# Optimization experiments

Hardware: AMD Instinct MI355X
Metric: run time of the kernel (lower is better)

Reference implementation:

```python
import jax, jax.numpy as jnp
import numpy as np

LEAKY = 0.1


def _leaky(x):
    return jnp.where(x > 0, x, LEAKY * x)


def _weightnet(d_xyz, ws):
    # d_xyz: [B,N,K,3]; ws: list of (w [Cin,Cout], b [Cout]) -> [B,N,K,W]
    h = d_xyz
    for w, b in ws:
        h = jax.nn.relu(jnp.einsum('bnki,io->bnko', h, w) + b)
    return h


def _gather(pts, idx):
    # pts: [B,M,C], idx: [B,N,K] -> [B,N,K,C]
    return jax.vmap(lambda p, i: p[i])(pts, idx)


def _cross(xyz1, xyz2, p1, p2, wn, lw, lb, nsample):
    # xyz1 [B,N1,3], xyz2 [B,N2,3], p1 [B,N1,D1], p2 [B,N2,D2]
    B, N1, _ = xyz1.shape
    # squared distances [B,N1,N2]
    d = (jnp.sum(xyz1 ** 2, -1)[:, :, None]
         + jnp.sum(xyz2 ** 2, -1)[:, None, :]
         - 2.0 * jnp.einsum('bnc,bmc->bnm', xyz1, xyz2))
    _, idx = jax.lax.top_k(-d, nsample)          # [B,N1,K] nearest
    neigh_xyz = _gather(xyz2, idx)               # [B,N1,K,3]
    direction = neigh_xyz - xyz1[:, :, None, :]  # [B,N1,K,3]
    gp2 = _gather(p2, idx)                       # [B,N1,K,D2]
    gp1 = jnp.broadcast_to(p1[:, :, None, :], (B, N1, nsample, p1.shape[-1]))
    new_pts = jnp.concatenate([gp1, gp2], axis=-1)   # [B,N1,K,D1+D2]
    w = _weightnet(direction, wn)                    # [B,N1,K,W]
    # [B,N1,D,K] @ [B,N1,K,W] -> [B,N1,D,W] -> flatten D-major (matches torch view)
    agg = jnp.einsum('bnkd,bnkw->bndw', new_pts, w).reshape(B, N1, -1)
    return _leaky(agg @ lw + lb)                     # [B,N1,out]


def setup_inputs() -> dict:
    key = jax.random.key(0)
    ks = jax.random.split(key, 20)
    B, N, C, MID, OUT, W = 4, 4096, 64, 128, 128, 16
    s = 0.05
    inp = {
        'pc1': jax.random.normal(ks[0], (B, 3, N), jnp.float32),
        'pc2': jax.random.normal(ks[1], (B, 3, N), jnp.float32),
        'feat1': jax.random.normal(ks[2], (B, C, N), jnp.float32),
        'feat2': jax.random.normal(ks[3], (B, C, N), jnp.float32),
        # WeightNet1: 3->8->8->16 pointwise linears (torch Conv2d 1x1), stored [Cin,Cout]
        'wn1_w0': jax.random.normal(ks[4], (3, 8), jnp.float32) * s,
        'wn1_b0': jnp.zeros((8,), jnp.float32),
        'wn1_w1': jax.random.normal(ks[5], (8, 8), jnp.float32) * s,
        'wn1_b1': jnp.zeros((8,), jnp.float32),
        'wn1_w2': jax.random.normal(ks[6], (8, W), jnp.float32) * s,
        'wn1_b2': jnp.zeros((W,), jnp.float32),
        'lin1_w': jax.random.normal(ks[7], (2 * C * W, MID), jnp.float32) * s,
        'lin1_b': jnp.zeros((MID,), jnp.float32),
        'wn2_w0': jax.random.normal(ks[8], (3, 8), jnp.float32) * s,
        'wn2_b0': jnp.zeros((8,), jnp.float32),
        'wn2_w1': jax.random.normal(ks[9], (8, 8), jnp.float32) * s,
        'wn2_b1': jnp.zeros((8,), jnp.float32),
        'wn2_w2': jax.random.normal(ks[10], (8, W), jnp.float32) * s,
        'wn2_b2': jnp.zeros((W,), jnp.float32),
        'lin2_w': jax.random.normal(ks[11], (2 * MID * W, OUT), jnp.float32) * s,
        'lin2_b': jnp.zeros((OUT,), jnp.float32),
    }
    return inp


def reference(pc1, pc2, feat1, feat2,
              wn1_w0, wn1_b0, wn1_w1, wn1_b1, wn1_w2, wn1_b2, lin1_w, lin1_b,
              wn2_w0, wn2_b0, wn2_w1, wn2_b1, wn2_w2, wn2_b2, lin2_w, lin2_b):
    nsample = 16
    wn1 = [(wn1_w0, wn1_b0), (wn1_w1, wn1_b1), (wn1_w2, wn1_b2)]
    wn2 = [(wn2_w0, wn2_b0), (wn2_w1, wn2_b1), (wn2_w2, wn2_b2)]
    x1 = pc1.transpose(0, 2, 1)   # [B,N,3]
    x2 = pc2.transpose(0, 2, 1)
    p1 = feat1.transpose(0, 2, 1)  # [B,N,C]
    p2 = feat2.transpose(0, 2, 1)
    f1n = _cross(x1, x2, p1, p2, wn1, lin1_w, lin1_b, nsample)   # [B,N1,mid]
    f2n = _cross(x2, x1, p2, p1, wn1, lin1_w, lin1_b, nsample)   # [B,N2,mid]
    f1f = _cross(x1, x2, f1n, f2n, wn2, lin2_w, lin2_b, nsample) # [B,N1,out]
    return (f1n.transpose(0, 2, 1), f2n.transpose(0, 2, 1), f1f.transpose(0, 2, 1))
```

## Files before the change

### kernel.cpp

```cpp
#include <hip/hip_runtime.h>
#include <hip/hip_bf16.h>
#include <cstddef>
#include <cstdint>

typedef __hip_bfloat16 bf16;
typedef __attribute__((ext_vector_type(8))) short bf16x8;
typedef __attribute__((ext_vector_type(4))) float f32x4;

#define NPT 4096
#define BB  4
#define NBR 16
#define WD  16
#define CDIM 64
#define MIDD 128

#define GLD16(g, l) __builtin_amdgcn_global_load_lds( \
    (const __attribute__((address_space(1))) unsigned int*)(const void*)(g), \
    (__attribute__((address_space(3))) unsigned int*)(void*)(l), 16, 0, 0)

__global__ __launch_bounds__(256)
void prep_kernel(const float* __restrict__ feat1, const float* __restrict__ feat2,
                 float* __restrict__ p1pm, bf16* __restrict__ p1b,
                 float* __restrict__ p2pm, bf16* __restrict__ p2b,
                 const float* __restrict__ lin1_w, bf16* __restrict__ b1hi, bf16* __restrict__ b1lo,
                 const float* __restrict__ lin2_w, bf16* __restrict__ b2hi, bf16* __restrict__ b2lo)
{
    __shared__ float t[32][33];
    const int tx = threadIdx.x & 31, ty = threadIdx.x >> 5;
    const int id = blockIdx.x;
    if (id < 2048) {
        const int which = id >> 10;
        const int nt = id & 1023;
        const int n0 = (nt & 127) * 32;
        const int c0 = ((nt >> 7) & 1) * 32;
        const int b  = nt >> 8;
        const float* in = which ? feat2 : feat1;
        float* out  = which ? p2pm : p1pm;
        bf16*  outb = which ? p2b  : p1b;
        #pragma unroll
        for (int r = ty; r < 32; r += 8)
            t[r][tx] = in[((size_t)b * CDIM + c0 + r) * NPT + n0 + tx];
        __syncthreads();
        #pragma unroll
        for (int r = ty; r < 32; r += 8) {
            const float v = t[tx][r];
            out [((size_t)b * NPT + n0 + r) * CDIM + c0 + tx] = v;
            outb[((size_t)b * NPT + n0 + r) * CDIM + c0 + tx] = __float2bfloat16(v);
        }
    } else {
        const float* w; bf16 *hi, *lo; int K, k0, o0;
        if (id < 2304) {
            const int id2 = id - 2048;
            w = lin1_w; hi = b1hi; lo = b1lo; K = 2048;
            k0 = (id2 & 63) * 32; o0 = (id2 >> 6) * 32;
        } else {
            const int id2 = id - 2304;
            w = lin2_w; hi = b2hi; lo = b2lo; K = 4096;
            k0 = (id2 & 127) * 32; o0 = (id2 >> 7) * 32;
        }
        #pragma unroll
        for (int r = ty; r < 32; r += 8)
            t[r][tx] = w[(size_t)(k0 + r) * MIDD + o0 + tx];
        __syncthreads();
        #pragma unroll
        for (int r = ty; r < 32; r += 8) {
            const float v = t[tx][r];
            const bf16 h = __float2bfloat16(v);
            const bf16 l2 = __float2bfloat16(v - __bfloat162float(h));
            hi[(size_t)(o0 + r) * K + k0 + tx] = h;
            lo[(size_t)(o0 + r) * K + k0 + tx] = l2;
        }
    }
}

#define KQ     16
#define KSEG   16
#define KCH    64
#define KSTAGE 1024
#define KRING  96

__global__ __launch_bounds__(256)
void knn_kernel(const float* __restrict__ pcA, const float* __restrict__ pcB,
                int* __restrict__ idxAB, int* __restrict__ idxBA)
{
    const float *qxyz, *cxyz; int* idx_out;
    if (blockIdx.z == 0) { qxyz = pcA; cxyz = pcB; idx_out = idxAB; }
    else                 { qxyz = pcB; cxyz = pcA; idx_out = idxBA; }

    __shared__ float4 cf[KSTAGE + KSTAGE / KCH];
    __shared__ float  pubd[2][KSEG][KQ];
    __shared__ float4 qc[KQ];
    __shared__ float  u16s[KQ];
    __shared__ int    rcnt[KQ];
    __shared__ int    wtot;
    __shared__ int    wl[256];
    __shared__ float  ringd[KQ][KRING + 1];
    __shared__ int    ringi[KQ][KRING + 1];

    const int tid = threadIdx.x;
    const int q   = tid & (KQ - 1);
    const int s   = tid >> 4;
    const int b   = blockIdx.y;
    const int n   = blockIdx.x * KQ + q;

    const float* qp = qxyz + (size_t)b * 3 * NPT;
    const float qx = qp[n], qy = qp[NPT + n], qz = qp[2 * NPT + n];
    const float q2 = fmaf(qx, qx, fmaf(qy, qy, qz * qz));
    const float* c = cxyz + (size_t)b * 3 * NPT;

    if (tid < KQ) rcnt[tid] = 0;
    if (tid == 0) wtot = 0;
    if (s == 0) qc[q] = make_float4(qx, qy, qz, q2);

    float b0 = 3.4e38f, b1 = 3.4e38f;
    int   i0 = 0;
    for (int st = 0; st < NPT; st += KSTAGE) {
        __syncthreads();
        {
            #pragma unroll
            for (int r = 0; r < KSTAGE / 256; ++r) {
                const int j = r * 256 + tid;
                const int g = st + j;
                const float x = c[g], y = c[NPT + g], z = c[2 * NPT + g];
                cf[j + (j >> 6)] = make_float4(x, y, z,
                    fmaf(x, x, fmaf(y, y, z * z)));
            }
        }
        __syncthreads();
        const int base = s * (KCH + 1);
        const int gidx = st + s * KCH;
        #pragma unroll 4
        for (int jj = 0; jj < KCH; ++jj) {
            const float4 pv = cf[base + jj];
            const float dot = fmaf(qx, pv.x, fmaf(qy, pv.y, qz * pv.z));
            const float d = q2 + pv.w - 2.f * dot;
            i0 = (d < b0) ? (gidx + jj) : i0;
            const float t = fmaxf(b0, d);
            b0 = fminf(b0, d);
            b1 = fminf(b1, t);
        }
    }
    pubd[0][s][q] = b0;
    pubd[1][s][q] = b1;
    __syncthreads();

    {
        float tv[32];
        #pragma unroll
        for (int j = 0; j < 32; ++j) tv[j] = pubd[j >> 4][j & 15][q];
        #pragma unroll
        for (int rep = 0; rep < 2; ++rep) {
            const int j = rep * 16 + s;
            const float vj = pubd[rep][s][q];
            int rank = 0;
            #pragma unroll
            for (int k = 0; k < 32; ++k)
                rank += (tv[k] < vj || (tv[k] == vj && k < j)) ? 1 : 0;
            if (rank == 15) u16s[q] = vj;
        }
    }
    __syncthreads();

    {
        const float gate = u16s[q];
        if (b0 <= gate) {
            if (b1 > gate) {
                const int slot = atomicAdd(&rcnt[q], 1);
                if (slot < KRING) { ringd[q][slot] = b0; ringi[q][slot] = i0; }
            } else {
                const int u = atomicAdd(&wtot, 1);
                wl[u] = (q << 4) | s;
            }
        }
    }
    __syncthreads();

    {
        const int W = wtot;
        const int lu = tid & 15;
        for (int u = tid >> 4; u < W; u += 16) {
            const int qq  = wl[u] >> 4;
            const int seg = wl[u] & 15;
            const float4 qv = qc[qq];
            const float gate = u16s[qq];
            #pragma unroll
            for (int ch = 0; ch < 4; ++ch) {
                const int j = ch * KSTAGE + seg * KCH + lu * 4;
                const float4 xs = *(const float4*)(c + j);
                const float4 ys = *(const float4*)(c + NPT + j);
                const float4 zs = *(const float4*)(c + 2 * NPT + j);
                const float xv[4] = { xs.x, xs.y, xs.z, xs.w };
                const float yv[4] = { ys.x, ys.y, ys.z, ys.w };
                const float zv[4] = { zs.x, zs.y, zs.z, zs.w };
                #pragma unroll
                for (int e = 0; e < 4; ++e) {
                    const float p2 = fmaf(xv[e], xv[e], fmaf(yv[e], yv[e], zv[e] * zv[e]));
                    const float dot = fmaf(qv.x, xv[e], fmaf(qv.y, yv[e], qv.z * zv[e]));
                    const float d = qv.w + p2 - 2.f * dot;
                    if (d <= gate) {
                        const int slot = atomicAdd(&rcnt[qq], 1);
                        if (slot < KRING) { ringd[qq][slot] = d; ringi[qq][slot] = j + e; }
                    }
                }
            }
        }
    }
    __syncthreads();

    {
        const int cnt = min(rcnt[q], KRING);
        int* op = idx_out + ((size_t)b * NPT + n) * NBR;
        for (int e = s; e < cnt; e += KSEG) {
            const float de = ringd[q][e];
            const int   ie = ringi[q][e];
            int rank = 0;
            for (int k = 0; k < cnt; ++k) {
                const float dk = ringd[q][k];
                const int   ik = ringi[q][k];
                rank += (dk < de || (dk == de && ik < ie)) ? 1 : 0;
            }
            if (rank < NBR) op[rank] = ie;
        }
    }
}

template<int D2, int PTS>
__global__ __launch_bounds__(256)
void agg_kernel(const float* __restrict__ qA, const float* __restrict__ cA,
                const bf16* __restrict__ nbrA, const int* __restrict__ idxA,
                const float* __restrict__ qB, const float* __restrict__ cB,
                const bf16* __restrict__ nbrB, const int* __restrict__ idxB,
                int Msplit,
                const float* __restrict__ w0, const float* __restrict__ b0,
                const float* __restrict__ w1, const float* __restrict__ b1,
                const float* __restrict__ w2, const float* __restrict__ b2,
                bf16* __restrict__ agg, float* __restrict__ swb, int m0)
{
    constexpr int TPP  = 256 / PTS;
    constexpr int ND   = D2 / TPP;
    constexpr int WSTR = 276;

    __shared__ float wp[248];
    __shared__ int   nb[PTS * NBR];
    __shared__ float wgt[PTS * WSTR];

    const int tid = threadIdx.x;
    const int mbase = m0 + (int)blockIdx.x * PTS;
    const bool second = mbase >= Msplit;
    const int mrow = second ? mbase - Msplit : mbase;
    const float* qxyz   = second ? qB   : qA;
    const float* cxyz   = second ? cB   : cA;
    const bf16*  nbr_b  = second ? nbrB : nbrA;
    const int*   idx    = second ? idxB : idxA;
    const int b = mrow >> 12;
    const int nbase = mrow & (NPT - 1);

    if (tid < 248) {
        float v;
        if      (tid <  24) v = w0[tid];
        else if (tid <  32) v = b0[tid - 24];
        else if (tid <  96) v = w1[tid - 32];
        else if (tid < 104) v = b1[tid - 96];
        else if (tid < 232) v = w2[tid - 104];
        else                v = b2[tid - 232];
        wp[tid] = v;
    }
    if (tid < PTS * NBR)
        nb[tid] = idx[(size_t)mrow * NBR + tid];
    __syncthreads();

    const int p  = tid & (PTS - 1);
    const int dg = tid / PTS;
    const int d0 = dg * ND;

    unsigned int F[NBR];
    {
        const bf16* base = nbr_b + (size_t)b * NPT * D2 + d0;
        #pragma unroll
        for (int k = 0; k < NBR; ++k) {
            const int j = nb[p * NBR + k];
            F[k] = *(const unsigned int*)(base + (size_t)j * D2);
        }
    }

    if (tid < PTS * NBR) {
        const int pp = tid / NBR, k = tid % NBR;
        const int n = nbase + pp;
        const int j = nb[tid];
        const float* q = qxyz + (size_t)b * 3 * NPT;
        const float* c = cxyz + (size_t)b * 3 * NPT;
        const float dx = c[j]           - q[n];
        const float dy = c[NPT + j]     - q[NPT + n];
        const float dz = c[2 * NPT + j] - q[2 * NPT + n];
        float h1[8], h2[8];
        #pragma unroll
        for (int o = 0; o < 8; ++o) {
            float v = wp[24 + o];
            v = fmaf(dx, wp[o], v);
            v = fmaf(dy, wp[8 + o], v);
            v = fmaf(dz, wp[16 + o], v);
            h1[o] = fmaxf(v, 0.f);
        }
        #pragma unroll
        for (int o = 0; o < 8; ++o) {
            float v = wp[96 + o];
            #pragma unroll
            for (int i = 0; i < 8; ++i) v = fmaf(h1[i], wp[32 + i * 8 + o], v);
            h2[o] = fmaxf(v, 0.f);
        }
        #pragma unroll
        for (int o = 0; o < WD; ++o) {
            float v = wp[232 + o];
            #pragma unroll
            for (int i = 0; i < 8; ++i) v = fmaf(h2[i], wp[104 + i * WD + o], v);
            wgt[pp * WSTR + k * WD + o] = fmaxf(v, 0.f);
        }
    }
    __syncthreads();

    if (tid < PTS * 16) {
        const int pp = tid >> 4, w = tid & 15;
        const float* wgp = wgt + pp * WSTR + w;
        float sv = 0.f;
        #pragma unroll
        for (int k = 0; k < NBR; ++k) sv += wgp[k * WD];
        swb[(size_t)((int)blockIdx.x * PTS + pp) * 16 + w] = sv;
    }

    {
        const float* wg = wgt + p * WSTR;
        bf16* aout = agg + ((size_t)((int)blockIdx.x * PTS + p)) * (2 * D2 * WD);
        float acc[ND][16];
        #pragma unroll
        for (int di = 0; di < ND; ++di)
            #pragma unroll
            for (int w = 0; w < 16; ++w) acc[di][w] = 0.f;
        #pragma unroll
        for (int k = 0; k < NBR; ++k) {
            union { unsigned int u; bf16 h[2]; } uf;
            uf.u = F[k];
            float Fv[ND];
            #pragma unroll
            for (int j = 0; j < ND; ++j) Fv[j] = __bfloat162float(uf.h[j]);
            const float4 v0 = *(const float4*)(wg + k * WD);
            const float4 v1 = *(const float4*)(wg + k * WD + 4);
            const float4 v2 = *(const float4*)(wg + k * WD + 8);
            const float4 v3 = *(const float4*)(wg + k * WD + 12);
            float w16[16];
            w16[0]  = v0.x; w16[1]  = v0.y; w16[2]  = v0.z; w16[3]  = v0.w;
            w16[4]  = v1.x; w16[5]  = v1.y; w16[6]  = v1.z; w16[7]  = v1.w;
            w16[8]  = v2.x; w16[9]  = v2.y; w16[10] = v2.z; w16[11] = v2.w;
            w16[12] = v3.x; w16[13] = v3.y; w16[14] = v3.z; w16[15] = v3.w;
            #pragma unroll
            for (int di = 0; di < ND; ++di)
                #pragma unroll
                for (int w = 0; w < 16; ++w)
                    acc[di][w] = fmaf(Fv[di], w16[w], acc[di][w]);
        }
        #pragma unroll
        for (int di = 0; di < ND; ++di) {
            union { bf16 h[16]; uint4 q[2]; } pk;
            #pragma unroll
            for (int w = 0; w < 16; ++w) pk.h[w] = __float2bfloat16(acc[di][w]);
            bf16* dst = aout + (D2 + d0 + di) * WD;
            *(uint4*)dst       = pk.q[0];
            *(uint4*)(dst + 8) = pk.q[1];
        }
    }
}

template<int BM>
__global__ __launch_bounds__(256)
void gemm_mfma(const bf16* __restrict__ A, const bf16* __restrict__ Bhi,
               const bf16* __restrict__ Blo, const float* __restrict__ bias,
               const float* __restrict__ ownf, const float* __restrict__ swb,
               float* __restrict__ out_t, float* __restrict__ out_pm,
               bf16* __restrict__ out_pmb, int m0, int K)
{
    constexpr int AE   = BM * 32;
    constexpr int BUFE = AE + 8192;
    constexpr int MF   = BM / 32;
    __shared__ __align__(16) char smem[2 * BUFE * 2];
    bf16* lds = (bf16*)smem;

    const int tid  = threadIdx.x;
    const int w    = tid >> 6;
    const int lane = tid & 63;
    const int wr   = w >> 1, wc = w & 1;
    const int mb   = (int)blockIdx.x * BM;
    const int gK   = lane >> 4;
    const int rL   = lane & 15;
    const int D2v  = K / 32;

    const int row_r = tid >> 2;
    const int row_s = row_r < BM ? row_r : BM - 1;
    const int ch_s  = tid & 3;
    const int sch_s = ch_s ^ ((row_s >> 1) & 3);
    const int w0_s  = (sch_s & 1) * 8;
    float sww[8];
    {
        const float* sp = swb + (size_t)(mb + row_s) * 16 + w0_s;
        const float4 a = *(const float4*)sp;
        const float4 b2 = *(const float4*)(sp + 4);
        sww[0] = a.x;  sww[1] = a.y;  sww[2] = a.z;  sww[3] = a.w;
        sww[4] = b2.x; sww[5] = b2.y; sww[6] = b2.z; sww[7] = b2.w;
    }
    const float* ownrow_g = ownf + (size_t)(m0 + mb + row_s) * D2v;

    f32x4 acc[MF][4];
    #pragma unroll
    for (int i = 0; i < MF; ++i)
        #pragma unroll
        for (int j = 0; j < 4; ++j) acc[i][j] = (f32x4)0.f;

    const int nk = K / 32;
    const int nkOwn = nk / 2;

    auto stage = [&](int buf, int kt) {
        const int kb = kt * 32;
        const int bufo = buf * BUFE;
        if (kt < nkOwn) {
            if (tid < BM * 4) {
                const int d = kt * 2 + (sch_s >> 1);
                const float f = ownrow_g[d];
                union { bf16 h[8]; uint4 q; } pk;
                #pragma unroll
                for (int j = 0; j < 8; ++j) pk.h[j] = __float2bfloat16(f * sww[j]);
                *(uint4*)(lds + bufo + tid * 8) = pk.q;
            }
        } else {
            if (w * 64 < BM * 4)
                GLD16(A + (size_t)(mb + row_r) * K + kb + (sch_s << 3),
                      lds + bufo + ((w * 64) << 3));
        }
        #pragma unroll
        for (int i = 0; i < 2; ++i) {
            const int s2 = i * 256 + tid;
            const int row = s2 >> 2, ch = s2 & 3;
            const int sch = ch ^ ((row >> 1) & 3);
            const int wb = (i * 256 + w * 64) << 3;
            GLD16(Bhi + (size_t)row * K + kb + (sch << 3), lds + bufo + AE + wb);
            GLD16(Blo + (size_t)row * K + kb + (sch << 3), lds + bufo + AE + 4096 + wb);
        }
    };

    stage(0, 0);
    __syncthreads();

    for (int kt = 0; kt < nk; ++kt) {
        const int cur = kt & 1;
        if (kt + 1 < nk) stage(cur ^ 1, kt + 1);

        const bf16* la  = lds + cur * BUFE;
        const bf16* lbh = la + AE;
        const bf16* lbl = la + AE + 4096;

        bf16x8 af[MF], bh[4], bl[4];
        #pragma unroll
        for (int mf = 0; mf < MF; ++mf) {
            const int row = wr * (BM / 2) + mf * 16 + rL;
            af[mf] = *(const bf16x8*)(la + row * 32 + ((gK ^ ((row >> 1) & 3)) << 3));
        }
        #pragma unroll
        for (int nf = 0; nf < 4; ++nf) {
            const int col = wc * 64 + nf * 16 + rL;
            const int off = col * 32 + ((gK ^ ((col >> 1) & 3)) << 3);
            bh[nf] = *(const bf16x8*)(lbh + off);
            bl[nf] = *(const bf16x8*)(lbl + off);
        }
        #pragma unroll
        for (int mf = 0; mf < MF; ++mf)
            #pragma unroll
            for (int nf = 0; nf < 4; ++nf) {
                acc[mf][nf] = __builtin_amdgcn_mfma_f32_16x16x32_bf16(af[mf], bh[nf], acc[mf][nf], 0, 0, 0);
                acc[mf][nf] = __builtin_amdgcn_mfma_f32_16x16x32_bf16(af[mf], bl[nf], acc[mf][nf], 0, 0, 0);
            }
        __syncthreads();
    }

    float (*tile)[133] = (float(*)[133])smem;
    #pragma unroll
    for (int mf = 0; mf < MF; ++mf)
        #pragma unroll
        for (int nf = 0; nf < 4; ++nf) {
            const int col = wc * 64 + nf * 16 + rL;
            const float bs = bias[col];
            #pragma unroll
            for (int qq = 0; qq < 4; ++qq) {
                const int rrow = wr * (BM / 2) + mf * 16 + gK * 4 + qq;
                const float v = acc[mf][nf][qq] + bs;
                tile[rrow][col] = v > 0.f ? v : 0.1f * v;
            }
        }
    __syncthreads();

    const int mrow = m0 + mb;
    const int b = mrow >> 12, n0 = mrow & (NPT - 1);
    for (int e = tid; e < BM * MIDD; e += 256) {
        const int o = e / BM, i = e % BM;
        out_t[((size_t)b * MIDD + o) * NPT + n0 + i] = tile[i][o];
    }
    if (out_pm) {
        for (int e = tid; e < BM * MIDD; e += 256) {
            const int i = e >> 7, o = e & 127;
            const float v = tile[i][o];
            out_pm [(size_t)(mrow + i) * MIDD + o] = v;
            out_pmb[(size_t)(mrow + i) * MIDD + o] = __float2bfloat16(v);
        }
    }
}

extern "C" void kernel_launch(void* const* d_in, const int* in_sizes, int n_in,
                              void* d_out, int out_size, void* d_ws, size_t ws_size,
                              hipStream_t stream)
{
    (void)in_sizes; (void)n_in; (void)out_size;
    const float* pc1    = (const float*)d_in[0];
    const float* pc2    = (const float*)d_in[1];
    const float* feat1  = (const float*)d_in[2];
    const float* feat2  = (const float*)d_in[3];
    const float* wn1_w0 = (const float*)d_in[4];
    const float* wn1_b0 = (const float*)d_in[5];
    const float* wn1_w1 = (const float*)d_in[6];
    const float* wn1_b1 = (const float*)d_in[7];
    const float* wn1_w2 = (const float*)d_in[8];
    const float* wn1_b2 = (const float*)d_in[9];
    const float* lin1_w = (const float*)d_in[10];
    const float* lin1_b = (const float*)d_in[11];
    const float* wn2_w0 = (const float*)d_in[12];
    const float* wn2_b0 = (const float*)d_in[13];
    const float* wn2_w1 = (const float*)d_in[14];
    const float* wn2_b1 = (const float*)d_in[15];
    const float* wn2_w2 = (const float*)d_in[16];
    const float* wn2_b2 = (const float*)d_in[17];
    const float* lin2_w = (const float*)d_in[18];
    const float* lin2_b = (const float*)d_in[19];
    float* out = (float*)d_out;

    const int M  = BB * NPT;
    const int M2 = 2 * M;
    const int K1 = 2 * CDIM * WD;
    const int K2 = 2 * MIDD * WD;

    char* ws = (char*)d_ws;
    float* p1pm = (float*)ws;
    float* p2pm = p1pm + (size_t)M * CDIM;
    float* fpm  = p2pm + (size_t)M * CDIM;
    bf16*  p1b  = (bf16*)(fpm + (size_t)M2 * MIDD);
    bf16*  p2b  = p1b + (size_t)M * CDIM;
    bf16*  fb   = p2b + (size_t)M * CDIM;
    int* idx12  = (int*)(fb + (size_t)M2 * MIDD);
    int* idx21  = idx12 + (size_t)M * NBR;
    bf16* b1hi  = (bf16*)(idx21 + (size_t)M * NBR);
    bf16* b1lo  = b1hi + (size_t)MIDD * K1;
    bf16* b2hi  = b1lo + (size_t)MIDD * K1;
    bf16* b2lo  = b2hi + (size_t)MIDD * K2;
    float* swbuf = (float*)(b2lo + (size_t)MIDD * K2);
    bf16* aggbuf = (bf16*)(swbuf + (size_t)(M2 + 64) * 16);
    const size_t used = (size_t)((char*)aggbuf - ws);
    const size_t avail = ws_size > used ? ws_size - used : 0;

    float* f1t = out;
    float* fft = out + 2 * (size_t)BB * MIDD * NPT;

    prep_kernel<<<2816, 256, 0, stream>>>(feat1, feat2, p1pm, p1b, p2pm, p2b,
                                          lin1_w, b1hi, b1lo, lin2_w, b2hi, b2lo);
    knn_kernel<<<dim3(NPT / KQ, BB, 2), 256, 0, stream>>>(pc1, pc2, idx12, idx21);

    auto chunk_rows = [&](int K) -> int {
        long rows = (long)(avail / ((size_t)K * sizeof(bf16)));
        int cm = (int)(rows > M2 ? M2 : rows) & ~127;
        if (cm < 128) cm = 128;
        return cm;
    };

    {
        const int CMr = chunk_rows(K1);
        for (int m0 = 0; m0 < M2; m0 += CMr) {
            const int cm = (M2 - m0 < CMr) ? (M2 - m0) : CMr;
            agg_kernel<CDIM, 8><<<cm / 8, 256, 0, stream>>>(
                pc1, pc2, p2b, idx12,
                pc2, pc1, p1b, idx21, M,
                wn1_w0, wn1_b0, wn1_w1, wn1_b1, wn1_w2, wn1_b2,
                aggbuf, swbuf, m0);
            gemm_mfma<64><<<cm / 64, 256, 0, stream>>>(aggbuf, b1hi, b1lo, lin1_b,
                                                       p1pm, swbuf,
                                                       f1t, fpm, fb, m0, K1);
        }
    }
    {
        const int CMr = chunk_rows(K2);
        for (int m0 = 0; m0 < M; m0 += CMr) {
            const int cm = (M - m0 < CMr) ? (M - m0) : CMr;
            agg_kernel<MIDD, 4><<<cm / 4, 256, 0, stream>>>(
                pc1, pc2, fb + (size_t)M * MIDD, idx12,
                nullptr, nullptr, nullptr, nullptr, M2,
                wn2_w0, wn2_b0, wn2_w1, wn2_b1, wn2_w2, wn2_b2,
                aggbuf, swbuf, m0);
            gemm_mfma<32><<<cm / 32, 256, 0, stream>>>(aggbuf, b2hi, b2lo, lin2_b,
                                                       fpm, swbuf,
                                                       fft, nullptr, nullptr, m0, K2);
        }
    }
}
```

Measured before the change: 316.1 us.

## Merge prep and kNN kernels into one launch; deepen GEMM K-tile to 64

The feature/weight transpose prep kernel and the kNN kernel become a single launch, with block-index ranges picking the role, so the two independent jobs can overlap and one launch is saved. The split-bf16 MFMA GEMM now stages 64-wide K tiles instead of 32, with an XOR swizzle over 8 chunks and two MFMA sub-steps per tile. This halves the number of barrier-separated k-iterations. In exchange it doubles the LDS footprint per buffer, which may reduce occupancy, and the fused kernel's shared memory now includes both roles' arrays.

```diff
diff --git a/kernel.cpp b/kernel.cpp
--- a/kernel.cpp
+++ b/kernel.cpp
@@ -18,61 +18,6 @@
     (const __attribute__((address_space(1))) unsigned int*)(const void*)(g), \
     (__attribute__((address_space(3))) unsigned int*)(void*)(l), 16, 0, 0)
 
-__global__ __launch_bounds__(256)
-void prep_kernel(const float* __restrict__ feat1, const float* __restrict__ feat2,
-                 float* __restrict__ p1pm, bf16* __restrict__ p1b,
-                 float* __restrict__ p2pm, bf16* __restrict__ p2b,
-                 const float* __restrict__ lin1_w, bf16* __restrict__ b1hi, bf16* __restrict__ b1lo,
-                 const float* __restrict__ lin2_w, bf16* __restrict__ b2hi, bf16* __restrict__ b2lo)
-{
-    __shared__ float t[32][33];
-    const int tx = threadIdx.x & 31, ty = threadIdx.x >> 5;
-    const int id = blockIdx.x;
-    if (id < 2048) {
-        const int which = id >> 10;
-        const int nt = id & 1023;
-        const int n0 = (nt & 127) * 32;
-        const int c0 = ((nt >> 7) & 1) * 32;
-        const int b  = nt >> 8;
-        const float* in = which ? feat2 : feat1;
-        float* out  = which ? p2pm : p1pm;
-        bf16*  outb = which ? p2b  : p1b;
-        #pragma unroll
-        for (int r = ty; r < 32; r += 8)
-            t[r][tx] = in[((size_t)b * CDIM + c0 + r) * NPT + n0 + tx];
-        __syncthreads();
-        #pragma unroll
-        for (int r = ty; r < 32; r += 8) {
-            const float v = t[tx][r];
-            out [((size_t)b * NPT + n0 + r) * CDIM + c0 + tx] = v;
-            outb[((size_t)b * NPT + n0 + r) * CDIM + c0 + tx] = __float2bfloat16(v);
-        }
-    } else {
-        const float* w; bf16 *hi, *lo; int K, k0, o0;
-        if (id < 2304) {
-            const int id2 = id - 2048;
-            w = lin1_w; hi = b1hi; lo = b1lo; K = 2048;
-            k0 = (id2 & 63) * 32; o0 = (id2 >> 6) * 32;
-        } else {
-            const int id2 = id - 2304;
-            w = lin2_w; hi = b2hi; lo = b2lo; K = 4096;
-            k0 = (id2 & 127) * 32; o0 = (id2 >> 7) * 32;
-        }
-        #pragma unroll
-        for (int r = ty; r < 32; r += 8)
-            t[r][tx] = w[(size_t)(k0 + r) * MIDD + o0 + tx];
-        __syncthreads();
-        #pragma unroll
-        for (int r = ty; r < 32; r += 8) {
-            const float v = t[tx][r];
-            const bf16 h = __float2bfloat16(v);
-            const bf16 l2 = __float2bfloat16(v - __bfloat162float(h));
-            hi[(size_t)(o0 + r) * K + k0 + tx] = h;
-            lo[(size_t)(o0 + r) * K + k0 + tx] = l2;
-        }
-    }
-}
-
 #define KQ     16
 #define KSEG   16
 #define KCH    64
@@ -80,13 +25,14 @@
 #define KRING  96
 
 __global__ __launch_bounds__(256)
-void knn_kernel(const float* __restrict__ pcA, const float* __restrict__ pcB,
-                int* __restrict__ idxAB, int* __restrict__ idxBA)
+void pre_kernel(const float* __restrict__ pcA, const float* __restrict__ pcB,
+                int* __restrict__ idxAB, int* __restrict__ idxBA,
+                const float* __restrict__ feat1, const float* __restrict__ feat2,
+                float* __restrict__ p1pm, bf16* __restrict__ p1b,
+                float* __restrict__ p2pm, bf16* __restrict__ p2b,
+                const float* __restrict__ lin1_w, bf16* __restrict__ b1hi, bf16* __restrict__ b1lo,
+                const float* __restrict__ lin2_w, bf16* __restrict__ b2hi, bf16* __restrict__ b2lo)
 {
-    const float *qxyz, *cxyz; int* idx_out;
-    if (blockIdx.z == 0) { qxyz = pcA; cxyz = pcB; idx_out = idxAB; }
-    else                 { qxyz = pcB; cxyz = pcA; idx_out = idxBA; }
-
     __shared__ float4 cf[KSTAGE + KSTAGE / KCH];
     __shared__ float  pubd[2][KSEG][KQ];
     __shared__ float4 qc[KQ];
@@ -96,130 +42,187 @@
     __shared__ int    wl[256];
     __shared__ float  ringd[KQ][KRING + 1];
     __shared__ int    ringi[KQ][KRING + 1];
-
+    __shared__ float  t[32][33];
+
+    const int bid = blockIdx.x;
     const int tid = threadIdx.x;
-    const int q   = tid & (KQ - 1);
-    const int s   = tid >> 4;
-    const int b   = blockIdx.y;
-    const int n   = blockIdx.x * KQ + q;
-
-    const float* qp = qxyz + (size_t)b * 3 * NPT;
-    const float qx = qp[n], qy = qp[NPT + n], qz = qp[2 * NPT + n];
-    const float q2 = fmaf(qx, qx, fmaf(qy, qy, qz * qz));
-    const float* c = cxyz + (size_t)b * 3 * NPT;
-
-    if (tid < KQ) rcnt[tid] = 0;
-    if (tid == 0) wtot = 0;
-    if (s == 0) qc[q] = make_float4(qx, qy, qz, q2);
-
-    float b0 = 3.4e38f, b1 = 3.4e38f;
-    int   i0 = 0;
-    for (int st = 0; st < NPT; st += KSTAGE) {
+
+    if (bid < 2048) {
+        const int dir = bid >> 10;
+        const int b   = (bid >> 8) & 3;
+        const int g   = bid & 255;
+        const float* qxyz = dir ? pcB : pcA;
+        const float* cxyz = dir ? pcA : pcB;
+        int* idx_out      = dir ? idxBA : idxAB;
+
+        const int q = tid & (KQ - 1);
+        const int s = tid >> 4;
+        const int n = g * KQ + q;
+
+        const float* qp = qxyz + (size_t)b * 3 * NPT;
+        const float qx = qp[n], qy = qp[NPT + n], qz = qp[2 * NPT + n];
+        const float q2 = fmaf(qx, qx, fmaf(qy, qy, qz * qz));
+        const float* c = cxyz + (size_t)b * 3 * NPT;
+
+        if (tid < KQ) rcnt[tid] = 0;
+        if (tid == 0) wtot = 0;
+        if (s == 0) qc[q] = make_float4(qx, qy, qz, q2);
+
+        float b0 = 3.4e38f, b1 = 3.4e38f;
+        int   i0 = 0;
+        for (int st = 0; st < NPT; st += KSTAGE) {
+            __syncthreads();
+            {
+                #pragma unroll
+                for (int r = 0; r < KSTAGE / 256; ++r) {
+                    const int j = r * 256 + tid;
+                    const int gg = st + j;
+                    const float x = c[gg], y = c[NPT + gg], z = c[2 * NPT + gg];
+                    cf[j + (j >> 6)] = make_float4(x, y, z,
+                        fmaf(x, x, fmaf(y, y, z * z)));
+                }
+            }
+            __syncthreads();
+            const int base = s * (KCH + 1);
+            const int gidx = st + s * KCH;
+            #pragma unroll 4
+            for (int jj = 0; jj < KCH; ++jj) {
+                const float4 pv = cf[base + jj];
+                const float dot = fmaf(qx, pv.x, fmaf(qy, pv.y, qz * pv.z));
+                const float d = q2 + pv.w - 2.f * dot;
+                i0 = (d < b0) ? (gidx + jj) : i0;
+                const float tt = fmaxf(b0, d);
+                b0 = fminf(b0, d);
+                b1 = fminf(b1, tt);
+            }
+        }
+        pubd[0][s][q] = b0;
+        pubd[1][s][q] = b1;
         __syncthreads();
+
         {
-            #pragma unroll
-            for (int r = 0; r < KSTAGE / 256; ++r) {
-                const int j = r * 256 + tid;
-                const int g = st + j;
-                const float x = c[g], y = c[NPT + g], z = c[2 * NPT + g];
-                cf[j + (j >> 6)] = make_float4(x, y, z,
-                    fmaf(x, x, fmaf(y, y, z * z)));
+            float tv[32];
+            #pragma unroll
+            for (int j = 0; j < 32; ++j) tv[j] = pubd[j >> 4][j & 15][q];
+            #pragma unroll
+            for (int rep = 0; rep < 2; ++rep) {
+                const int j = rep * 16 + s;
+                const float vj = pubd[rep][s][q];
+                int rank = 0;
+                #pragma unroll
+                for (int k = 0; k < 32; ++k)
+                    rank += (tv[k] < vj || (tv[k] == vj && k < j)) ? 1 : 0;
+                if (rank == 15) u16s[q] = vj;
             }
         }
         __syncthreads();
-        const int base = s * (KCH + 1);
-        const int gidx = st + s * KCH;
-        #pragma unroll 4
-        for (int jj = 0; jj < KCH; ++jj) {
-            const float4 pv = cf[base + jj];
-            const float dot = fmaf(qx, pv.x, fmaf(qy, pv.y, qz * pv.z));
-            const float d = q2 + pv.w - 2.f * dot;
-            i0 = (d < b0) ? (gidx + jj) : i0;
-            const float t = fmaxf(b0, d);
-            b0 = fminf(b0, d);
-            b1 = fminf(b1, t);
-        }
-    }
-    pubd[0][s][q] = b0;
-    pubd[1][s][q] = b1;
-    __syncthreads();
-
-    {
-        float tv[32];
-        #pragma unroll
-        for (int j = 0; j < 32; ++j) tv[j] = pubd[j >> 4][j & 15][q];
-        #pragma unroll
-        for (int rep = 0; rep < 2; ++rep) {
-            const int j = rep * 16 + s;
-            const float vj = pubd[rep][s][q];
-            int rank = 0;
-            #pragma unroll
-            for (int k = 0; k < 32; ++k)
-                rank += (tv[k] < vj || (tv[k] == vj && k < j)) ? 1 : 0;
-            if (rank == 15) u16s[q] = vj;
-        }
-    }
-    __syncthreads();
-
-    {
-        const float gate = u16s[q];
-        if (b0 <= gate) {
-            if (b1 > gate) {
-                const int slot = atomicAdd(&rcnt[q], 1);
-                if (slot < KRING) { ringd[q][slot] = b0; ringi[q][slot] = i0; }
-            } else {
-                const int u = atomicAdd(&wtot, 1);
-                wl[u] = (q << 4) | s;
-            }
-        }
-    }
-    __syncthreads();
-
-    {
-        const int W = wtot;
-        const int lu = tid & 15;
-        for (int u = tid >> 4; u < W; u += 16) {
-            const int qq  = wl[u] >> 4;
-            const int seg = wl[u] & 15;
-            const float4 qv = qc[qq];
-            const float gate = u16s[qq];
-            #pragma unroll
-            for (int ch = 0; ch < 4; ++ch) {
-                const int j = ch * KSTAGE + seg * KCH + lu * 4;
-                const float4 xs = *(const float4*)(c + j);
-                const float4 ys = *(const float4*)(c + NPT + j);
-                const float4 zs = *(const float4*)(c + 2 * NPT + j);
-                const float xv[4] = { xs.x, xs.y, xs.z, xs.w };
-                const float yv[4] = { ys.x, ys.y, ys.z, ys.w };
-                const float zv[4] = { zs.x, zs.y, zs.z, zs.w };
+
+        {
+            const float gate = u16s[q];
+            if (b0 <= gate) {
+                if (b1 > gate) {
+                    const int slot = atomicAdd(&rcnt[q], 1);
+                    if (slot < KRING) { ringd[q][slot] = b0; ringi[q][slot] = i0; }
+                } else {
+                    const int u = atomicAdd(&wtot, 1);
+                    wl[u] = (q << 4) | s;
+                }
+            }
+        }
+        __syncthreads();
+
+        {
+            const int W = wtot;
+            const int lu = tid & 15;
+            for (int u = tid >> 4; u < W; u += 16) {
+                const int qq  = wl[u] >> 4;
+                const int seg = wl[u] & 15;
+                const float4 qv = qc[qq];
+                const float gate = u16s[qq];
                 #pragma unroll
-                for (int e = 0; e < 4; ++e) {
-                    const float p2 = fmaf(xv[e], xv[e], fmaf(yv[e], yv[e], zv[e] * zv[e]));
-                    const float dot = fmaf(qv.x, xv[e], fmaf(qv.y, yv[e], qv.z * zv[e]));
-                    const float d = qv.w + p2 - 2.f * dot;
-                    if (d <= gate) {
-                        const int slot = atomicAdd(&rcnt[qq], 1);
-                        if (slot < KRING) { ringd[qq][slot] = d; ringi[qq][slot] = j + e; }
+                for (int ch = 0; ch < 4; ++ch) {
+                    const int j = ch * KSTAGE + seg * KCH + lu * 4;
+                    const float4 xs = *(const float4*)(c + j);
+                    const float4 ys = *(const float4*)(c + NPT + j);
+                    const float4 zs = *(const float4*)(c + 2 * NPT + j);
+                    const float xv[4] = { xs.x, xs.y, xs.z, xs.w };
+                    const float yv[4] = { ys.x, ys.y, ys.z, ys.w };
+                    const float zv[4] = { zs.x, zs.y, zs.z, zs.w };
+                    #pragma unroll
+                    for (int e = 0; e < 4; ++e) {
+                        const float p2 = fmaf(xv[e], xv[e], fmaf(yv[e], yv[e], zv[e] * zv[e]));
+                        const float dot = fmaf(qv.x, xv[e], fmaf(qv.y, yv[e], qv.z * zv[e]));
+                        const float d = qv.w + p2 - 2.f * dot;
+                        if (d <= gate) {
+                            const int slot = atomicAdd(&rcnt[qq], 1);
+                            if (slot < KRING) { ringd[qq][slot] = d; ringi[qq][slot] = j + e; }
+                        }
                     }
                 }
             }
         }
-    }
-    __syncthreads();
-
-    {
-        const int cnt = min(rcnt[q], KRING);
-        int* op = idx_out + ((size_t)b * NPT + n) * NBR;
-        for (int e = s; e < cnt; e += KSEG) {
-            const float de = ringd[q][e];
-            const int   ie = ringi[q][e];
-            int rank = 0;
-            for (int k = 0; k < cnt; ++k) {
-                const float dk = ringd[q][k];
-                const int   ik = ringi[q][k];
-                rank += (dk < de || (dk == de && ik < ie)) ? 1 : 0;
-            }
-            if (rank < NBR) op[rank] = ie;
+        __syncthreads();
+
+        {
+            const int cnt = min(rcnt[q], KRING);
+            int* op = idx_out + ((size_t)b * NPT + n) * NBR;
+            for (int e = s; e < cnt; e += KSEG) {
+                const float de = ringd[q][e];
+                const int   ie = ringi[q][e];
+                int rank = 0;
+                for (int k = 0; k < cnt; ++k) {
+                    const float dk = ringd[q][k];
+                    const int   ik = ringi[q][k];
+                    rank += (dk < de || (dk == de && ik < ie)) ? 1 : 0;
+                }
+                if (rank < NBR) op[rank] = ie;
+            }
+        }
+    } else {
+        const int tx = tid & 31, ty = tid >> 5;
+        const int id = bid - 2048;
+        if (id < 2048) {
+            const int which = id >> 10;
+            const int nt = id & 1023;
+            const int n0 = (nt & 127) * 32;
+            const int c0 = ((nt >> 7) & 1) * 32;
+            const int b  = nt >> 8;
+            const float* in = which ? feat2 : feat1;
+            float* out  = which ? p2pm : p1pm;
+            bf16*  outb = which ? p2b  : p1b;
+            #pragma unroll
+            for (int r = ty; r < 32; r += 8)
+                t[r][tx] = in[((size_t)b * CDIM + c0 + r) * NPT + n0 + tx];
+            __syncthreads();
+            #pragma unroll
+            for (int r = ty; r < 32; r += 8) {
+                const float v = t[tx][r];
+                out [((size_t)b * NPT + n0 + r) * CDIM + c0 + tx] = v;
+                outb[((size_t)b * NPT + n0 + r) * CDIM + c0 + tx] = __float2bfloat16(v);
+            }
+        } else {
+            const float* w; bf16 *hi, *lo; int K, k0, o0;
+            if (id < 2304) {
+                const int id2 = id - 2048;
+                w = lin1_w; hi = b1hi; lo = b1lo; K = 2048;
+                k0 = (id2 & 63) * 32; o0 = (id2 >> 6) * 32;
+            } else {
+                const int id2 = id - 2304;
+                w = lin2_w; hi = b2hi; lo = b2lo; K = 4096;
+                k0 = (id2 & 127) * 32; o0 = (id2 >> 7) * 32;
+            }
+            #pragma unroll
+            for (int r = ty; r < 32; r += 8)
+                t[r][tx] = w[(size_t)(k0 + r) * MIDD + o0 + tx];
+            __syncthreads();
+            #pragma unroll
+            for (int r = ty; r < 32; r += 8) {
+                const float v = t[tx][r];
+                const bf16 h = __float2bfloat16(v);
+                const bf16 l2 = __float2bfloat16(v - __bfloat162float(h));
+                hi[(size_t)(o0 + r) * K + k0 + tx] = h;
+                lo[(size_t)(o0 + r) * K + k0 + tx] = l2;
+            }
         }
     }
 }
@@ -371,15 +374,17 @@
 
 template<int BM>
 __global__ __launch_bounds__(256)
-void gemm_mfma(const bf16* __restrict__ A, const bf16* __restrict__ Bhi,
-               const bf16* __restrict__ Blo, const float* __restrict__ bias,
-               const float* __restrict__ ownf, const float* __restrict__ swb,
-               float* __restrict__ out_t, float* __restrict__ out_pm,
-               bf16* __restrict__ out_pmb, int m0, int K)
+void gemm_mfma_k64(const bf16* __restrict__ A, const bf16* __restrict__ Bhi,
+                   const bf16* __restrict__ Blo, const float* __restrict__ bias,
+                   const float* __restrict__ ownf, const float* __restrict__ swb,
+                   float* __restrict__ out_t, float* __restrict__ out_pm,
+                   bf16* __restrict__ out_pmb, int m0, int K)
 {
-    constexpr int AE   = BM * 32;
-    constexpr int BUFE = AE + 8192;
+    constexpr int AE   = BM * 64;
+    constexpr int BT   = 128 * 64;
+    constexpr int BUFE = AE + 2 * BT;
     constexpr int MF   = BM / 32;
+    constexpr int RA   = BM * 8 / 256;
     __shared__ __align__(16) char smem[2 * BUFE * 2];
     bf16* lds = (bf16*)smem;
 
@@ -392,20 +397,23 @@
     const int rL   = lane & 15;
     const int D2v  = K / 32;
 
-    const int row_r = tid >> 2;
-    const int row_s = row_r < BM ? row_r : BM - 1;
-    const int ch_s  = tid & 3;
-    const int sch_s = ch_s ^ ((row_s >> 1) & 3);
-    const int w0_s  = (sch_s & 1) * 8;
-    float sww[8];
-    {
-        const float* sp = swb + (size_t)(mb + row_s) * 16 + w0_s;
+    int rowA[RA], schA[RA];
+    float sww[RA][8];
+    const float* ownrow_g[RA];
+    #pragma unroll
+    for (int r = 0; r < RA; ++r) {
+        const int slot = r * 256 + tid;
+        rowA[r] = slot >> 3;
+        const int ch = slot & 7;
+        schA[r] = ch ^ (rowA[r] & 7);
+        const int w0 = (schA[r] & 1) * 8;
+        const float* sp = swb + (size_t)(mb + rowA[r]) * 16 + w0;
         const float4 a = *(const float4*)sp;
         const float4 b2 = *(const float4*)(sp + 4);
-        sww[0] = a.x;  sww[1] = a.y;  sww[2] = a.z;  sww[3] = a.w;
-        sww[4] = b2.x; sww[5] = b2.y; sww[6] = b2.z; sww[7] = b2.w;
-    }
-    const float* ownrow_g = ownf + (size_t)(m0 + mb + row_s) * D2v;
+        sww[r][0] = a.x;  sww[r][1] = a.y;  sww[r][2] = a.z;  sww[r][3] = a.w;
+        sww[r][4] = b2.x; sww[r][5] = b2.y; sww[r][6] = b2.z; sww[r][7] = b2.w;
+        ownrow_g[r] = ownf + (size_t)(m0 + mb + rowA[r]) * D2v;
+    }
 
     f32x4 acc[MF][4];
     #pragma unroll
@@ -413,34 +421,36 @@
         #pragma unroll
         for (int j = 0; j < 4; ++j) acc[i][j] = (f32x4)0.f;
 
-    const int nk = K / 32;
+    const int nk = K / 64;
     const int nkOwn = nk / 2;
 
     auto stage = [&](int buf, int kt) {
-        const int kb = kt * 32;
+        const int kb = kt * 64;
         const int bufo = buf * BUFE;
         if (kt < nkOwn) {
-            if (tid < BM * 4) {
-                const int d = kt * 2 + (sch_s >> 1);
-                const float f = ownrow_g[d];
+            #pragma unroll
+            for (int r = 0; r < RA; ++r) {
+                const int d = kt * 4 + (schA[r] >> 1);
+                const float f = ownrow_g[r][d];
                 union { bf16 h[8]; uint4 q; } pk;
                 #pragma unroll
-                for (int j = 0; j < 8; ++j) pk.h[j] = __float2bfloat16(f * sww[j]);
-                *(uint4*)(lds + bufo + tid * 8) = pk.q;
+                for (int j = 0; j < 8; ++j) pk.h[j] = __float2bfloat16(f * sww[r][j]);
+                *(uint4*)(lds + bufo + (r * 256 + tid) * 8) = pk.q;
             }
         } else {
-            if (w * 64 < BM * 4)
-                GLD16(A + (size_t)(mb + row_r) * K + kb + (sch_s << 3),
-                      lds + bufo + ((w * 64) << 3));
-        }
-        #pragma unroll
-        for (int i = 0; i < 2; ++i) {
+            #pragma unroll
+            for (int r = 0; r < RA; ++r)
+                GLD16(A + (size_t)(mb + rowA[r]) * K + kb + (schA[r] << 3),
+                      lds + bufo + ((r * 256 + w * 64) << 3));
+        }
+        #pragma unroll
+        for (int i = 0; i < 4; ++i) {
             const int s2 = i * 256 + tid;
-            const int row = s2 >> 2, ch = s2 & 3;
-            const int sch = ch ^ ((row >> 1) & 3);
+            const int row = s2 >> 3, ch = s2 & 7;
+            const int sch = ch ^ (row & 7);
             const int wb = (i * 256 + w * 64) << 3;
             GLD16(Bhi + (size_t)row * K + kb + (sch << 3), lds + bufo + AE + wb);
-            GLD16(Blo + (size_t)row * K + kb + (sch << 3), lds + bufo + AE + 4096 + wb);
+            GLD16(Blo + (size_t)row * K + kb + (sch << 3), lds + bufo + AE + BT + wb);
         }
     };
 
@@ -453,28 +463,32 @@
 
         const bf16* la  = lds + cur * BUFE;
         const bf16* lbh = la + AE;
-        const bf16* lbl = la + AE + 4096;
-
-        bf16x8 af[MF], bh[4], bl[4];
-        #pragma unroll
-        for (int mf = 0; mf < MF; ++mf) {
-            const int row = wr * (BM / 2) + mf * 16 + rL;
-            af[mf] = *(const bf16x8*)(la + row * 32 + ((gK ^ ((row >> 1) & 3)) << 3));
-        }
-        #pragma unroll
-        for (int nf = 0; nf < 4; ++nf) {
-            const int col = wc * 64 + nf * 16 + rL;
-            const int off = col * 32 + ((gK ^ ((col >> 1) & 3)) << 3);
-            bh[nf] = *(const bf16x8*)(lbh + off);
-            bl[nf] = *(const bf16x8*)(lbl + off);
-        }
-        #pragma unroll
-        for (int mf = 0; mf < MF; ++mf)
+        const bf16* lbl = la + AE + BT;
+
+        #pragma unroll
+        for (int kk2 = 0; kk2 < 2; ++kk2) {
+            const int cc = gK + kk2 * 4;
+            bf16x8 af[MF], bh[4], bl[4];
+            #pragma unroll
+            for (int mf = 0; mf < MF; ++mf) {
+                const int row = wr * (BM / 2) + mf * 16 + rL;
+                af[mf] = *(const bf16x8*)(la + row * 64 + ((cc ^ (row & 7)) << 3));
+            }
             #pragma unroll
             for (int nf = 0; nf < 4; ++nf) {
-                acc[mf][nf] = __builtin_amdgcn_mfma_f32_16x16x32_bf16(af[mf], bh[nf], acc[mf][nf], 0, 0, 0);
-                acc[mf][nf] = __builtin_amdgcn_mfma_f32_16x16x32_bf16(af[mf], bl[nf], acc[mf][nf], 0, 0, 0);
-            }
+                const int col = wc * 64 + nf * 16 + rL;
+                const int off = col * 64 + ((cc ^ (col & 7)) << 3);
+                bh[nf] = *(const bf16x8*)(lbh + off);
+                bl[nf] = *(const bf16x8*)(lbl + off);
+            }
+            #pragma unroll
+            for (int mf = 0; mf < MF; ++mf)
+                #pragma unroll
+                for (int nf = 0; nf < 4; ++nf) {
+                    acc[mf][nf] = __builtin_amdgcn_mfma_f32_16x16x32_bf16(af[mf], bh[nf], acc[mf][nf], 0, 0, 0);
+                    acc[mf][nf] = __builtin_amdgcn_mfma_f32_16x16x32_bf16(af[mf], bl[nf], acc[mf][nf], 0, 0, 0);
+                }
+        }
         __syncthreads();
     }
 
@@ -563,9 +577,10 @@
     float* f1t = out;
     float* fft = out + 2 * (size_t)BB * MIDD * NPT;
 
-    prep_kernel<<<2816, 256, 0, stream>>>(feat1, feat2, p1pm, p1b, p2pm, p2b,
-                                          lin1_w, b1hi, b1lo, lin2_w, b2hi, b2lo);
-    knn_kernel<<<dim3(NPT / KQ, BB, 2), 256, 0, stream>>>(pc1, pc2, idx12, idx21);
+    pre_kernel<<<2048 + 2816, 256, 0, stream>>>(
+        pc1, pc2, idx12, idx21,
+        feat1, feat2, p1pm, p1b, p2pm, p2b,
+        lin1_w, b1hi, b1lo, lin2_w, b2hi, b2lo);
 
     auto chunk_rows = [&](int K) -> int {
         long rows = (long)(avail / ((size_t)K * sizeof(bf16)));
@@ -583,9 +598,9 @@
                 pc2, pc1, p1b, idx21, M,
                 wn1_w0, wn1_b0, wn1_w1, wn1_b1, wn1_w2, wn1_b2,
                 aggbuf, swbuf, m0);
-            gemm_mfma<64><<<cm / 64, 256, 0, stream>>>(aggbuf, b1hi, b1lo, lin1_b,
-                                                       p1pm, swbuf,
-                                                       f1t, fpm, fb, m0, K1);
+            gemm_mfma_k64<64><<<cm / 64, 256, 0, stream>>>(aggbuf, b1hi, b1lo, lin1_b,
+                                                           p1pm, swbuf,
+                                                           f1t, fpm, fb, m0, K1);
         }
     }
     {
@@ -597,9 +612,9 @@
                 nullptr, nullptr, nullptr, nullptr, M2,
                 wn2_w0, wn2_b0, wn2_w1, wn2_b1, wn2_w2, wn2_b2,
                 aggbuf, swbuf, m0);
-            gemm_mfma<32><<<cm / 32, 256, 0, stream>>>(aggbuf, b2hi, b2lo, lin2_b,
-                                                       fpm, swbuf,
-                                                       fft, nullptr, nullptr, m0, K2);
+            gemm_mfma_k64<32><<<cm / 32, 256, 0, stream>>>(aggbuf, b2hi, b2lo, lin2_b,
+                                                           fpm, swbuf,
+                                                           fft, nullptr, nullptr, m0, K2);
         }
     }
 }
```

After: 277.5 us. -12.2%, faster.
